# Optimization experiments

Hardware: AMD Instinct MI355X
Metric: run time of the kernel (lower is better)

## Reference

```python
import jax, jax.numpy as jnp
import numpy as np

N_NODES = 50000
N_EDGES = 1600000
HIDDEN = 256
N_GRAPHS = 1024
N_PROPS = 8
N_FEAT = 4
IN_DIM = N_FEAT + 4 * 8 + 4 * 8  # 68


def setup_inputs() -> dict:
    key = jax.random.key(0)
    ks = jax.random.split(key, 20)
    s = 0.05
    inp = {
        "x": jax.random.randint(ks[0], (N_NODES, N_FEAT), 0, 720),
        "edge_index": jax.random.randint(ks[1], (2, N_EDGES), 0, N_NODES),
        "batch": jnp.sort(jax.random.randint(ks[2], (N_NODES,), 0, N_GRAPHS)),
        "emb24": jax.random.normal(ks[3], (24, 8), jnp.float32) * s,
        "emb72": jax.random.normal(ks[4], (72, 8), jnp.float32) * s,
        "lin1_w": jax.random.normal(ks[5], (HIDDEN, IN_DIM), jnp.float32) * s,
        "lin1_b": jnp.zeros((HIDDEN,), jnp.float32),
        "qa1_w": jax.random.normal(ks[6], (HIDDEN, HIDDEN), jnp.float32) * s,
        "qa1_b": jnp.zeros((HIDDEN,), jnp.float32),
        "lin2_w": jax.random.normal(ks[7], (HIDDEN, HIDDEN), jnp.float32) * s,
        "lin2_b": jnp.zeros((HIDDEN,), jnp.float32),
        "qa2_w": jax.random.normal(ks[8], (HIDDEN, HIDDEN), jnp.float32) * s,
        "qa2_b": jnp.zeros((HIDDEN,), jnp.float32),
        "head_w1": jax.random.normal(ks[9], (N_PROPS, HIDDEN // 2, HIDDEN), jnp.float32) * s,
        "head_b1": jnp.zeros((N_PROPS, HIDDEN // 2), jnp.float32),
        "head_w2": jax.random.normal(ks[10], (N_PROPS, 1, HIDDEN // 2), jnp.float32) * s,
        "head_b2": jnp.zeros((N_PROPS, 1), jnp.float32),
    }
    return inp


def _qagcn_conv(h, src, dst, lin_w, lin_b, qa_w, qa_b):
    n = h.shape[0]
    lin_x = h @ lin_w.T + lin_b                                  # [N, H]
    # message = lin(x_j); aggr='add' over edges; add_self_loops contributes
    # one extra lin_x per node, and update() adds lin(x) again -> 2*lin_x.
    aggr = jax.ops.segment_sum(lin_x[src], dst, num_segments=n)  # [N, H]
    h2 = aggr + 2.0 * lin_x
    b, e, _, _ = jnp.split(h2, 4, axis=-1)
    h3 = jnp.concatenate([b, e, b + e, b + 2.0 * e], axis=-1)
    return jax.nn.relu(h3 @ qa_w.T + qa_b)


def reference(x, edge_index, batch, emb24, emb72, lin1_w, lin1_b, qa1_w, qa1_b,
              lin2_w, lin2_b, qa2_w, qa2_b, head_w1, head_b1, head_w2, head_b2):
    n = x.shape[0]
    r24 = emb24[x % 24].reshape(n, -1)          # [N, 32]
    r72 = emb72[x % 72].reshape(n, -1)          # [N, 32]
    h = jnp.concatenate([x.astype(jnp.float32), r24, r72], axis=-1)  # [N, 68]
    src, dst = edge_index[0], edge_index[1]
    h = _qagcn_conv(h, src, dst, lin1_w, lin1_b, qa1_w, qa1_b)
    h = _qagcn_conv(h, src, dst, lin2_w, lin2_b, qa2_w, qa2_b)
    # global mean pool over graphs
    sums = jax.ops.segment_sum(h, batch, num_segments=N_GRAPHS)      # [G, H]
    cnts = jax.ops.segment_sum(jnp.ones((n,), h.dtype), batch, num_segments=N_GRAPHS)
    g = sums / jnp.maximum(cnts, 1.0)[:, None]                       # [G, H]
    # per-property 2-layer MLP heads
    h1 = jax.nn.relu(jnp.einsum('gd,phd->pgh', g, head_w1) + head_b1[:, None, :])
    out = jnp.einsum('pgh,poh->pgo', h1, head_w2) + head_b2[:, None, :]  # [P, G, 1]
    return out[..., 0].T                                             # [G, P]
```

## Files before the change

kernel.cpp:

```cpp
#include <hip/hip_runtime.h>
#include <hip/hip_bf16.h>

#define N_NODESC 50000
#define N_EDGESC 1600000
#define NGC 1024
#define NPC 8
#define NBIN 196
#define NBLKE 391

typedef __attribute__((ext_vector_type(8))) short bf16x8;
typedef __attribute__((ext_vector_type(4))) float f32x4;

__device__ inline ushort f2bf(float f) {
  union { float f; uint u; } v; v.f = f;
  uint u = v.u;
  u += 0x7FFF + ((u >> 16) & 1);
  return (ushort)(u >> 16);
}
__device__ inline float bflo(uint u) {
  union { uint u; float f; } v; v.u = u << 16; return v.f;
}
__device__ inline float bfhi(uint u) {
  union { uint u; float f; } v; v.u = u & 0xFFFF0000u; return v.f;
}

__global__ __launch_bounds__(256) void megaprep(
    const float* __restrict__ qa1w, const float* __restrict__ qa2w,
    const float* __restrict__ lin1w, const float* __restrict__ lin2w,
    ushort* __restrict__ qe1, ushort* __restrict__ qe2,
    ushort* __restrict__ l1w, ushort* __restrict__ l2w,
    const int* __restrict__ x, const float* __restrict__ e24,
    const float* __restrict__ e72, ushort* __restrict__ feat,
    const int* __restrict__ dst, int* __restrict__ bh) {
  int bid = blockIdx.x, t = threadIdx.x;
  if (bid < 256) {
    const float* qw = (bid < 128) ? qa1w : qa2w;
    ushort* eff = (bid < 128) ? qe1 : qe2;
    int k = (bid & 127) * 2 + (t >> 7);
    int j = t & 127;
    const float* r = qw + (size_t)k * 256;
    float v;
    if (j < 64) v = r[j] + r[128 + j] + r[192 + j];
    else { int j2 = j - 64; v = r[64 + j2] + r[128 + j2] + 2.0f * r[192 + j2]; }
    eff[(size_t)k * 128 + j] = f2bf(v);
  } else if (bid < 304) {
    int i = (bid - 256) * 256 + t;
    int r = i / 96, c = i - r * 96;
    l1w[i] = (c < 68) ? f2bf(lin1w[(size_t)r * 68 + c]) : (ushort)0;
  } else if (bid < 432) {
    int r = bid - 304;
    l2w[(size_t)r * 256 + t] = f2bf(lin2w[(size_t)r * 256 + t]);
  } else if (bid < 1456) {
    const int stride = 1024 * 256;
    for (int i = (bid - 432) * 256 + t; i < N_NODESC * 96; i += stride) {
      int n = i / 96, tt = i - n * 96;
      float v = 0.f;
      if (tt < 4) v = (float)x[n * 4 + tt];
      else if (tt < 36) { int kk = tt - 4;  int f = kk >> 3, c = kk & 7; v = e24[(x[n * 4 + f] % 24) * 8 + c]; }
      else if (tt < 68) { int kk = tt - 36; int f = kk >> 3, c = kk & 7; v = e72[(x[n * 4 + f] % 72) * 8 + c]; }
      feat[i] = f2bf(v);
    }
  } else {
    __shared__ int hist[NBIN];
    int blk = bid - 1456;
    if (t < NBIN) hist[t] = 0;
    __syncthreads();
    int base = blk * 4096;
#pragma unroll
    for (int i = 0; i < 16; ++i) {
      int idx = base + i * 256 + t;
      if (idx < N_EDGESC) atomicAdd(&hist[dst[idx] >> 8], 1);
    }
    __syncthreads();
    if (t < NBIN) bh[(size_t)t * NBLKE + blk] = hist[t];
  }
}

__global__ __launch_bounds__(64) void csr_scan_bins(int* __restrict__ bh, int* __restrict__ bt) {
  int bin = blockIdx.x;
  int lane = threadIdx.x;
  int carry = 0;
  int* row = bh + (size_t)bin * NBLKE;
  for (int c = 0; c < NBLKE; c += 64) {
    int j = c + lane;
    int v = (j < NBLKE) ? row[j] : 0;
    int incl = v;
#pragma unroll
    for (int off = 1; off < 64; off <<= 1) {
      int u = __shfl_up(incl, off, 64);
      if (lane >= off) incl += u;
    }
    if (j < NBLKE) row[j] = carry + incl - v;
    carry += __shfl(incl, 63, 64);
  }
  if (lane == 0) bt[bin] = carry;
}

template <int K, int ASPLIT, int CSPLIT>
__device__ __forceinline__ void gemm_body(ushort* ws, int bx, int by,
    const ushort* __restrict__ A, const ushort* __restrict__ W,
    const float* __restrict__ bias, ushort* __restrict__ C,
    int M, int NC, int relu) {
  int tid = threadIdx.x;
  int lane = tid & 63;
  int wv = tid >> 6;
  int rbase = bx * 128 + wv * 32;
  int colt = by * 128;
  int r16 = lane & 15;
  int kg = (lane >> 4) * 8;

  const char* wt = (const char*)(W + (size_t)colt * K);
#pragma unroll
  for (int i = 0; i < K / 16; ++i) {
    int o = (i * 256 + tid) * 16;
    int col = o / (2 * K);
    int sw = o ^ ((col & 7) << 4);
    *(bf16x8*)((char*)ws + sw) = *(const bf16x8*)(wt + o);
  }
  __syncthreads();

  f32x4 acc[2][8];
#pragma unroll
  for (int m = 0; m < 2; ++m)
#pragma unroll
    for (int n = 0; n < 8; ++n) acc[m][n] = (f32x4){0.f, 0.f, 0.f, 0.f};

  for (int k0 = 0; k0 < K; k0 += 32) {
    int ks = k0 + kg;
    bf16x8 a[2], b[8];
#pragma unroll
    for (int m = 0; m < 2; ++m) {
      int rr = rbase + m * 16 + r16;
      if (rr >= M) rr = M - 1;
      const ushort* ap = ASPLIT ? (A + ((size_t)(ks >> 6) * N_NODESC + rr) * 64 + (ks & 63))
                                : (A + (size_t)rr * K + ks);
      a[m] = *(const bf16x8*)ap;
    }
#pragma unroll
    for (int n = 0; n < 8; ++n) {
      int cl = n * 16 + r16;
      int byte = (cl * 2 * K + ks * 2) ^ ((cl & 7) << 4);
      b[n] = *(const bf16x8*)((const char*)ws + byte);
    }
#pragma unroll
    for (int m = 0; m < 2; ++m)
#pragma unroll
      for (int n = 0; n < 8; ++n)
        acc[m][n] = __builtin_amdgcn_mfma_f32_16x16x32_bf16(a[m], b[n], acc[m][n], 0, 0, 0);
  }

  int rowoff = (lane >> 4) * 4;
#pragma unroll
  for (int m = 0; m < 2; ++m) {
#pragma unroll
    for (int j = 0; j < 4; ++j) {
      int row = rbase + m * 16 + rowoff + j;
      if (row >= M) continue;
#pragma unroll
      for (int n = 0; n < 8; ++n) {
        int col = colt + n * 16 + r16;
        float v = acc[m][n][j] + bias[col];
        if (relu) v = fmaxf(v, 0.f);
        size_t idx = CSPLIT ? ((size_t)(col >> 6) * N_NODESC + row) * 64 + (col & 63)
                            : (size_t)row * NC + col;
        C[idx] = f2bf(v);
      }
    }
  }
}

template <int K, int ASPLIT, int CSPLIT>
__global__ __launch_bounds__(256, 2) void mfma_gemm_lds(
    const ushort* __restrict__ A, const ushort* __restrict__ W,
    const float* __restrict__ bias, ushort* __restrict__ C,
    int M, int NC, int relu) {
  __shared__ ushort ws[128 * K];
  gemm_body<K, ASPLIT, CSPLIT>(ws, blockIdx.x, blockIdx.y, A, W, bias, C, M, NC, relu);
}

__global__ __launch_bounds__(256, 2) void scatter_lin1(
    const int* __restrict__ src, const int* __restrict__ dst,
    const int* __restrict__ bh, const int* __restrict__ bt, uint* __restrict__ tmp,
    const ushort* __restrict__ feat, const ushort* __restrict__ l1w,
    const float* __restrict__ lin1b, ushort* __restrict__ linx) {
  __shared__ ushort ws[128 * 96];
  int bid = blockIdx.x, t = threadIdx.x;
  if (bid < NBLKE) {
    int* sc = (int*)ws;
    int* cur = sc + 256;
    int v = (t < NBIN) ? bt[t] : 0;
    sc[t] = v;
    __syncthreads();
    for (int off = 1; off < 256; off <<= 1) {
      int u = (t >= off) ? sc[t - off] : 0;
      __syncthreads();
      sc[t] += u;
      __syncthreads();
    }
    if (t < NBIN) cur[t] = (sc[t] - v) + bh[(size_t)t * NBLKE + bid];
    __syncthreads();
    int base = bid * 4096;
#pragma unroll
    for (int i = 0; i < 16; ++i) {
      int idx = base + i * 256 + t;
      if (idx < N_EDGESC) {
        int d = dst[idx];
        uint p = ((uint)d << 16) | (uint)src[idx];
        int pos = atomicAdd(&cur[d >> 8], 1);
        tmp[pos] = p;
      }
    }
  } else {
    gemm_body<96, 0, 1>(ws, bid - NBLKE, 0, feat, l1w, lin1b, linx, N_NODESC, 128, 0);
  }
}

__global__ __launch_bounds__(256) void csr_bucket_sort(const uint* __restrict__ tmp,
                                                       const int* __restrict__ bt,
                                                       ushort* __restrict__ elist,
                                                       int* __restrict__ rp) {
  __shared__ int sc[256];
  __shared__ int cnt[256];
  int b = blockIdx.x, t = threadIdx.x;
  int v = (t < NBIN) ? bt[t] : 0;
  sc[t] = v;
  __syncthreads();
  for (int off = 1; off < 256; off <<= 1) {
    int u = (t >= off) ? sc[t - off] : 0;
    __syncthreads();
    sc[t] += u;
    __syncthreads();
  }
  int base = (b == 0) ? 0 : sc[b - 1];
  int end = sc[b];
  int total = sc[NBIN - 1];
  __syncthreads();
  cnt[t] = 0;
  __syncthreads();
  for (int i = base + t; i < end; i += 256)
    atomicAdd(&cnt[(tmp[i] >> 16) & 255], 1);
  __syncthreads();
  int cv = cnt[t];
  sc[t] = cv;
  __syncthreads();
  for (int off = 1; off < 256; off <<= 1) {
    int u = (t >= off) ? sc[t - off] : 0;
    __syncthreads();
    sc[t] += u;
    __syncthreads();
  }
  int excl = sc[t] - cv;
  int node = (b << 8) + t;
  if (node < N_NODESC) rp[node] = base + excl;
  if (b == NBIN - 1 && t == 0) rp[N_NODESC] = total;
  cnt[t] = base + excl;
  __syncthreads();
  for (int i = base + t; i < end; i += 256) {
    uint p = tmp[i];
    int pos = atomicAdd(&cnt[(p >> 16) & 255], 1);
    elist[pos] = (ushort)(p & 0xFFFFu);
  }
}

__global__ __launch_bounds__(256) void aggregate_h(const uint* __restrict__ lx,
                                                   const int* __restrict__ rp,
                                                   const ushort* __restrict__ elist,
                                                   uint* __restrict__ h2) {
  const int BPP = N_NODESC / 4;
  int bid = blockIdx.x;
  int pass = bid / BPP;
  int nb = bid - pass * BPP;
  const uint* T = lx + (size_t)pass * N_NODESC * 32;
  uint* O = h2 + (size_t)pass * N_NODESC * 32;
  int wv = threadIdx.x >> 6, lane = threadIdx.x & 63;
  int half = lane >> 5, c = lane & 31;
  int n = nb * 4 + wv;
  int beg = rp[n], end = rp[n + 1];
  float a0 = 0.f, a1 = 0.f;
  int e = beg + half;
  for (; e + 14 < end; e += 16) {
    int s0 = elist[e], s1 = elist[e + 2], s2 = elist[e + 4], s3 = elist[e + 6];
    int s4 = elist[e + 8], s5 = elist[e + 10], s6 = elist[e + 12], s7 = elist[e + 14];
    uint u0 = T[(size_t)s0 * 32 + c];
    uint u1 = T[(size_t)s1 * 32 + c];
    uint u2 = T[(size_t)s2 * 32 + c];
    uint u3 = T[(size_t)s3 * 32 + c];
    uint u4 = T[(size_t)s4 * 32 + c];
    uint u5 = T[(size_t)s5 * 32 + c];
    uint u6 = T[(size_t)s6 * 32 + c];
    uint u7 = T[(size_t)s7 * 32 + c];
    a0 += bflo(u0) + bflo(u1) + bflo(u2) + bflo(u3);
    a1 += bfhi(u0) + bfhi(u1) + bfhi(u2) + bfhi(u3);
    a0 += bflo(u4) + bflo(u5) + bflo(u6) + bflo(u7);
    a1 += bfhi(u4) + bfhi(u5) + bfhi(u6) + bfhi(u7);
  }
  for (; e < end; e += 2) {
    uint u = T[(size_t)elist[e] * 32 + c];
    a0 += bflo(u);
    a1 += bfhi(u);
  }
  a0 += __shfl_xor(a0, 32);
  a1 += __shfl_xor(a1, 32);
  if (half == 0) {
    uint su = T[(size_t)n * 32 + c];
    O[(size_t)n * 32 + c] = (uint)f2bf(a0 + 2.f * bflo(su)) |
                            ((uint)f2bf(a1 + 2.f * bfhi(su)) << 16);
  }
}

__global__ __launch_bounds__(256) void pool2(const uint* __restrict__ h,
                                             const int* __restrict__ batch,
                                             float* __restrict__ g) {
  int gg = blockIdx.x;
  int t = threadIdx.x;
  int j = t & 127, rg = t >> 7;
  int lo = 0, hi = N_NODESC;
  while (lo < hi) { int mid = (lo + hi) >> 1; if (batch[mid] < gg) lo = mid + 1; else hi = mid; }
  int beg = lo;
  hi = N_NODESC;
  while (lo < hi) { int mid = (lo + hi) >> 1; if (batch[mid] < gg + 1) lo = mid + 1; else hi = mid; }
  int end = lo;
  float a0 = 0.f, a1 = 0.f;
  int n = beg + rg;
  for (; n + 2 < end; n += 4) {
    uint u = h[(size_t)n * 128 + j];
    uint u2 = h[(size_t)(n + 2) * 128 + j];
    a0 += bflo(u) + bflo(u2);
    a1 += bfhi(u) + bfhi(u2);
  }
  if (n < end) {
    uint u = h[(size_t)n * 128 + j];
    a0 += bflo(u);
    a1 += bfhi(u);
  }
  __shared__ float s0[128], s1[128];
  if (rg == 1) { s0[j] = a0; s1[j] = a1; }
  __syncthreads();
  if (rg == 0) {
    a0 += s0[j];
    a1 += s1[j];
    float cfac = fmaxf((float)(end - beg), 1.0f);
    g[(size_t)gg * 256 + 2 * j] = a0 / cfac;
    g[(size_t)gg * 256 + 2 * j + 1] = a1 / cfac;
  }
}

__global__ __launch_bounds__(128) void head_kernel(const float* __restrict__ g,
    const float* __restrict__ w1, const float* __restrict__ b1,
    const float* __restrict__ w2, const float* __restrict__ b2,
    float* __restrict__ out) {
  int p = blockIdx.y;
  int g0 = blockIdx.x * 8;
  int t = threadIdx.x;
  __shared__ float gs[8][256];
  for (int i = t; i < 8 * 256; i += 128)
    gs[i >> 8][i & 255] = g[(size_t)(g0 + (i >> 8)) * 256 + (i & 255)];
  __syncthreads();
  const float4* w4 = (const float4*)(w1 + ((size_t)p * 128 + t) * 256);
  float bv = b1[p * 128 + t];
  float acc[8];
#pragma unroll
  for (int q = 0; q < 8; ++q) acc[q] = bv;
  for (int d4 = 0; d4 < 64; ++d4) {
    float4 wv = w4[d4];
#pragma unroll
    for (int q = 0; q < 8; ++q) {
      acc[q] += gs[q][d4 * 4 + 0] * wv.x + gs[q][d4 * 4 + 1] * wv.y +
                gs[q][d4 * 4 + 2] * wv.z + gs[q][d4 * 4 + 3] * wv.w;
    }
  }
  float w2v = w2[p * 128 + t];
  __shared__ float red[2][8];
  int wave = t >> 6, lane = t & 63;
#pragma unroll
  for (int q = 0; q < 8; ++q) {
    float v = fmaxf(acc[q], 0.f) * w2v;
    for (int o = 32; o > 0; o >>= 1) v += __shfl_down(v, o, 64);
    if (lane == 0) red[wave][q] = v;
  }
  __syncthreads();
  if (t < 8) out[(size_t)(g0 + t) * 8 + p] = red[0][t] + red[1][t] + b2[p];
}

extern "C" void kernel_launch(void* const* d_in, const int* in_sizes, int n_in,
                              void* d_out, int out_size, void* d_ws, size_t ws_size,
                              hipStream_t stream) {
  const int*   x     = (const int*)d_in[0];
  const int*   ei    = (const int*)d_in[1];
  const int*   batch = (const int*)d_in[2];
  const float* emb24 = (const float*)d_in[3];
  const float* emb72 = (const float*)d_in[4];
  const float* lin1w = (const float*)d_in[5];
  const float* lin1b = (const float*)d_in[6];
  const float* qa1w  = (const float*)d_in[7];
  const float* qa1b  = (const float*)d_in[8];
  const float* lin2w = (const float*)d_in[9];
  const float* lin2b = (const float*)d_in[10];
  const float* qa2w  = (const float*)d_in[11];
  const float* qa2b  = (const float*)d_in[12];
  const float* hw1   = (const float*)d_in[13];
  const float* hb1   = (const float*)d_in[14];
  const float* hw2   = (const float*)d_in[15];
  const float* hb2   = (const float*)d_in[16];
  float* out = (float*)d_out;

  const int* srcv = ei;
  const int* dstv = ei + N_EDGESC;

  char* wsb = (char*)d_ws;
  size_t off = 0;
  auto alloc = [&](size_t b) { char* p = wsb + off; off += (b + 255) & ~(size_t)255; return p; };
  ushort* feat  = (ushort*)alloc((size_t)N_NODESC * 96 * 2);
  ushort* linx  = (ushort*)alloc((size_t)N_NODESC * 128 * 2);
  ushort* h2    = (ushort*)alloc((size_t)N_NODESC * 128 * 2);
  ushort* h     = (ushort*)alloc((size_t)N_NODESC * 256 * 2);
  float*  gbuf  = (float*)alloc((size_t)NGC * 256 * 4);
  ushort* qe1   = (ushort*)alloc(256 * 128 * 2);
  ushort* qe2   = (ushort*)alloc(256 * 128 * 2);
  ushort* l1w   = (ushort*)alloc(128 * 96 * 2);
  ushort* l2w   = (ushort*)alloc(128 * 256 * 2);
  int*    rp    = (int*)alloc((size_t)(N_NODESC + 1) * 4);
  ushort* elist = (ushort*)alloc((size_t)N_EDGESC * 2);
  int*    bh    = (int*)alloc((size_t)NBIN * NBLKE * 4);
  int*    bt    = (int*)alloc((size_t)NBIN * 4);
  uint*   tmp   = (uint*)h;

  megaprep<<<1847, 256, 0, stream>>>(qa1w, qa2w, lin1w, lin2w, qe1, qe2, l1w, l2w,
                                     x, emb24, emb72, feat, dstv, bh);
  csr_scan_bins<<<NBIN, 64, 0, stream>>>(bh, bt);

  int gm = (N_NODESC + 127) / 128;

  scatter_lin1<<<NBLKE + gm, 256, 0, stream>>>(srcv, dstv, bh, bt, tmp,
                                               feat, l1w, lin1b, linx);
  csr_bucket_sort<<<NBIN, 256, 0, stream>>>(tmp, bt, elist, rp);

  aggregate_h<<<(N_NODESC / 4) * 2, 256, 0, stream>>>((const uint*)linx, rp, elist, (uint*)h2);
  mfma_gemm_lds<128, 1, 0><<<dim3(gm, 2), 256, 0, stream>>>(h2, qe1, qa1b, h, N_NODESC, 256, 1);

  mfma_gemm_lds<256, 0, 1><<<dim3(gm, 1), 256, 0, stream>>>(h, l2w, lin2b, linx, N_NODESC, 128, 0);
  aggregate_h<<<(N_NODESC / 4) * 2, 256, 0, stream>>>((const uint*)linx, rp, elist, (uint*)h2);
  mfma_gemm_lds<128, 1, 0><<<dim3(gm, 2), 256, 0, stream>>>(h2, qe2, qa2b, h, N_NODESC, 256, 1);

  pool2<<<NGC, 256, 0, stream>>>((const uint*)h, batch, gbuf);
  head_kernel<<<dim3(NGC / 8, NPC), 128, 0, stream>>>(gbuf, hw1, hb1, hw2, hb2, out);
}
```

Before: 288.7 us.

## Switch lin_x to row-major layout and aggregate all 128 columns per pass

The split 64-column planar layout of the lin_x and aggregate buffers is replaced with plain row-major layout in the GEMMs. The two-pass aggregation kernel becomes a single pass where each lane gathers a uint2 (4 bf16 values) per neighbour. This halves the number of edge-list reads and index loads and makes each gathered row one contiguous 256-byte segment. Edge-index loads are also marked nontemporal. The cost is more registers per thread and a larger per-pass working set for the gathered table.

```diff
diff --git a/kernel.cpp b/kernel.cpp
--- a/kernel.cpp
+++ b/kernel.cpp
@@ -96,7 +96,7 @@
   if (lane == 0) bt[bin] = carry;
 }
 
-template <int K, int ASPLIT, int CSPLIT>
+template <int K>
 __device__ __forceinline__ void gemm_body(ushort* ws, int bx, int by,
     const ushort* __restrict__ A, const ushort* __restrict__ W,
     const float* __restrict__ bias, ushort* __restrict__ C,
@@ -132,9 +132,7 @@
     for (int m = 0; m < 2; ++m) {
       int rr = rbase + m * 16 + r16;
       if (rr >= M) rr = M - 1;
-      const ushort* ap = ASPLIT ? (A + ((size_t)(ks >> 6) * N_NODESC + rr) * 64 + (ks & 63))
-                                : (A + (size_t)rr * K + ks);
-      a[m] = *(const bf16x8*)ap;
+      a[m] = *(const bf16x8*)(A + (size_t)rr * K + ks);
     }
 #pragma unroll
     for (int n = 0; n < 8; ++n) {
@@ -161,21 +159,19 @@
         int col = colt + n * 16 + r16;
         float v = acc[m][n][j] + bias[col];
         if (relu) v = fmaxf(v, 0.f);
-        size_t idx = CSPLIT ? ((size_t)(col >> 6) * N_NODESC + row) * 64 + (col & 63)
-                            : (size_t)row * NC + col;
-        C[idx] = f2bf(v);
+        C[(size_t)row * NC + col] = f2bf(v);
       }
     }
   }
 }
 
-template <int K, int ASPLIT, int CSPLIT>
+template <int K>
 __global__ __launch_bounds__(256, 2) void mfma_gemm_lds(
     const ushort* __restrict__ A, const ushort* __restrict__ W,
     const float* __restrict__ bias, ushort* __restrict__ C,
     int M, int NC, int relu) {
   __shared__ ushort ws[128 * K];
-  gemm_body<K, ASPLIT, CSPLIT>(ws, blockIdx.x, blockIdx.y, A, W, bias, C, M, NC, relu);
+  gemm_body<K>(ws, blockIdx.x, blockIdx.y, A, W, bias, C, M, NC, relu);
 }
 
 __global__ __launch_bounds__(256, 2) void scatter_lin1(
@@ -211,7 +207,7 @@
       }
     }
   } else {
-    gemm_body<96, 0, 1>(ws, bid - NBLKE, 0, feat, l1w, lin1b, linx, N_NODESC, 128, 0);
+    gemm_body<96>(ws, bid - NBLKE, 0, feat, l1w, lin1b, linx, N_NODESC, 128, 0);
   }
 }
 
@@ -262,49 +258,60 @@
   }
 }
 
-__global__ __launch_bounds__(256) void aggregate_h(const uint* __restrict__ lx,
+__global__ __launch_bounds__(256) void aggregate_v(const uint2* __restrict__ lx,
                                                    const int* __restrict__ rp,
                                                    const ushort* __restrict__ elist,
-                                                   uint* __restrict__ h2) {
-  const int BPP = N_NODESC / 4;
-  int bid = blockIdx.x;
-  int pass = bid / BPP;
-  int nb = bid - pass * BPP;
-  const uint* T = lx + (size_t)pass * N_NODESC * 32;
-  uint* O = h2 + (size_t)pass * N_NODESC * 32;
+                                                   uint2* __restrict__ h2) {
   int wv = threadIdx.x >> 6, lane = threadIdx.x & 63;
   int half = lane >> 5, c = lane & 31;
-  int n = nb * 4 + wv;
+  int n = blockIdx.x * 4 + wv;
   int beg = rp[n], end = rp[n + 1];
-  float a0 = 0.f, a1 = 0.f;
+  float a0 = 0.f, a1 = 0.f, a2 = 0.f, a3 = 0.f;
   int e = beg + half;
   for (; e + 14 < end; e += 16) {
-    int s0 = elist[e], s1 = elist[e + 2], s2 = elist[e + 4], s3 = elist[e + 6];
-    int s4 = elist[e + 8], s5 = elist[e + 10], s6 = elist[e + 12], s7 = elist[e + 14];
-    uint u0 = T[(size_t)s0 * 32 + c];
-    uint u1 = T[(size_t)s1 * 32 + c];
-    uint u2 = T[(size_t)s2 * 32 + c];
-    uint u3 = T[(size_t)s3 * 32 + c];
-    uint u4 = T[(size_t)s4 * 32 + c];
-    uint u5 = T[(size_t)s5 * 32 + c];
-    uint u6 = T[(size_t)s6 * 32 + c];
-    uint u7 = T[(size_t)s7 * 32 + c];
-    a0 += bflo(u0) + bflo(u1) + bflo(u2) + bflo(u3);
-    a1 += bfhi(u0) + bfhi(u1) + bfhi(u2) + bfhi(u3);
-    a0 += bflo(u4) + bflo(u5) + bflo(u6) + bflo(u7);
-    a1 += bfhi(u4) + bfhi(u5) + bfhi(u6) + bfhi(u7);
+    int s0 = __builtin_nontemporal_load(elist + e);
+    int s1 = __builtin_nontemporal_load(elist + e + 2);
+    int s2 = __builtin_nontemporal_load(elist + e + 4);
+    int s3 = __builtin_nontemporal_load(elist + e + 6);
+    int s4 = __builtin_nontemporal_load(elist + e + 8);
+    int s5 = __builtin_nontemporal_load(elist + e + 10);
+    int s6 = __builtin_nontemporal_load(elist + e + 12);
+    int s7 = __builtin_nontemporal_load(elist + e + 14);
+    uint2 u0 = lx[(size_t)s0 * 32 + c];
+    uint2 u1 = lx[(size_t)s1 * 32 + c];
+    uint2 u2 = lx[(size_t)s2 * 32 + c];
+    uint2 u3 = lx[(size_t)s3 * 32 + c];
+    uint2 u4 = lx[(size_t)s4 * 32 + c];
+    uint2 u5 = lx[(size_t)s5 * 32 + c];
+    uint2 u6 = lx[(size_t)s6 * 32 + c];
+    uint2 u7 = lx[(size_t)s7 * 32 + c];
+    a0 += bflo(u0.x) + bflo(u1.x) + bflo(u2.x) + bflo(u3.x);
+    a1 += bfhi(u0.x) + bfhi(u1.x) + bfhi(u2.x) + bfhi(u3.x);
+    a2 += bflo(u0.y) + bflo(u1.y) + bflo(u2.y) + bflo(u3.y);
+    a3 += bfhi(u0.y) + bfhi(u1.y) + bfhi(u2.y) + bfhi(u3.y);
+    a0 += bflo(u4.x) + bflo(u5.x) + bflo(u6.x) + bflo(u7.x);
+    a1 += bfhi(u4.x) + bfhi(u5.x) + bfhi(u6.x) + bfhi(u7.x);
+    a2 += bflo(u4.y) + bflo(u5.y) + bflo(u6.y) + bflo(u7.y);
+    a3 += bfhi(u4.y) + bfhi(u5.y) + bfhi(u6.y) + bfhi(u7.y);
   }
   for (; e < end; e += 2) {
-    uint u = T[(size_t)elist[e] * 32 + c];
-    a0 += bflo(u);
-    a1 += bfhi(u);
+    int s = __builtin_nontemporal_load(elist + e);
+    uint2 u = lx[(size_t)s * 32 + c];
+    a0 += bflo(u.x);
+    a1 += bfhi(u.x);
+    a2 += bflo(u.y);
+    a3 += bfhi(u.y);
   }
   a0 += __shfl_xor(a0, 32);
   a1 += __shfl_xor(a1, 32);
+  a2 += __shfl_xor(a2, 32);
+  a3 += __shfl_xor(a3, 32);
   if (half == 0) {
-    uint su = T[(size_t)n * 32 + c];
-    O[(size_t)n * 32 + c] = (uint)f2bf(a0 + 2.f * bflo(su)) |
-                            ((uint)f2bf(a1 + 2.f * bfhi(su)) << 16);
+    uint2 su = lx[(size_t)n * 32 + c];
+    uint2 w;
+    w.x = (uint)f2bf(a0 + 2.f * bflo(su.x)) | ((uint)f2bf(a1 + 2.f * bfhi(su.x)) << 16);
+    w.y = (uint)f2bf(a2 + 2.f * bflo(su.y)) | ((uint)f2bf(a3 + 2.f * bfhi(su.y)) << 16);
+    h2[(size_t)n * 32 + c] = w;
   }
 }
 
@@ -435,12 +442,12 @@
                                                feat, l1w, lin1b, linx);
   csr_bucket_sort<<<NBIN, 256, 0, stream>>>(tmp, bt, elist, rp);
 
-  aggregate_h<<<(N_NODESC / 4) * 2, 256, 0, stream>>>((const uint*)linx, rp, elist, (uint*)h2);
-  mfma_gemm_lds<128, 1, 0><<<dim3(gm, 2), 256, 0, stream>>>(h2, qe1, qa1b, h, N_NODESC, 256, 1);
-
-  mfma_gemm_lds<256, 0, 1><<<dim3(gm, 1), 256, 0, stream>>>(h, l2w, lin2b, linx, N_NODESC, 128, 0);
-  aggregate_h<<<(N_NODESC / 4) * 2, 256, 0, stream>>>((const uint*)linx, rp, elist, (uint*)h2);
-  mfma_gemm_lds<128, 1, 0><<<dim3(gm, 2), 256, 0, stream>>>(h2, qe2, qa2b, h, N_NODESC, 256, 1);
+  aggregate_v<<<N_NODESC / 4, 256, 0, stream>>>((const uint2*)linx, rp, elist, (uint2*)h2);
+  mfma_gemm_lds<128><<<dim3(gm, 2), 256, 0, stream>>>(h2, qe1, qa1b, h, N_NODESC, 256, 1);
+
+  mfma_gemm_lds<256><<<dim3(gm, 1), 256, 0, stream>>>(h, l2w, lin2b, linx, N_NODESC, 128, 0);
+  aggregate_v<<<N_NODESC / 4, 256, 0, stream>>>((const uint2*)linx, rp, elist, (uint2*)h2);
+  mfma_gemm_lds<128><<<dim3(gm, 2), 256, 0, stream>>>(h2, qe2, qa2b, h, N_NODESC, 256, 1);
 
   pool2<<<NGC, 256, 0, stream>>>((const uint*)h, batch, gbuf);
   head_kernel<<<dim3(NGC / 8, NPC), 128, 0, stream>>>(gbuf, hw1, hb1, hw2, hb2, out);
```

After: 266.5 us. -7.7%, faster.
